# Optimization experiments

Measured on AMD Instinct MI355X. Metric: run time of the kernel, lower is better.

## Reference

```python
import jax, jax.numpy as jnp
import numpy as np

N_NODES = 50000
N_EDGES = 640000
IN_DIM, HID_DIM, OUT_DIM = 128, 128, 64


def setup_inputs() -> dict:
    key = jax.random.key(0)
    k = jax.random.split(key, 6)
    x = jax.random.normal(k[0], (N_NODES, IN_DIM), dtype=jnp.float32)
    edge_index = jax.random.randint(k[1], (2, N_EDGES), 0, N_NODES, dtype=jnp.int64)
    edge_weight = jax.random.uniform(k[2], (N_EDGES,), dtype=jnp.float32)
    W1 = jax.random.normal(k[3], (IN_DIM, HID_DIM), dtype=jnp.float32) / np.sqrt(IN_DIM)
    b1 = jnp.zeros((HID_DIM,), dtype=jnp.float32)
    W2 = jax.random.normal(k[4], (HID_DIM, OUT_DIM), dtype=jnp.float32) / np.sqrt(HID_DIM)
    b2 = jnp.zeros((OUT_DIM,), dtype=jnp.float32)
    return {"x": x, "edge_index": edge_index, "edge_weight": edge_weight,
            "W1": W1, "b1": b1, "W2": W2, "b2": b2}


def _gcn_norm(edge_index, edge_weight, num_nodes):
    # PyG gcn_norm: add self-loops (weight 1.0), then deg^-1/2 * w * deg^-1/2.
    loop = jnp.arange(num_nodes, dtype=edge_index.dtype)
    row = jnp.concatenate([edge_index[0], loop])
    col = jnp.concatenate([edge_index[1], loop])
    w = jnp.concatenate([edge_weight, jnp.ones((num_nodes,), edge_weight.dtype)])
    deg = jax.ops.segment_sum(w, col, num_segments=num_nodes)  # in-degree (flow source->target)
    dinv = jnp.where(deg > 0, jax.lax.rsqrt(deg), 0.0)
    norm = dinv[row] * w * dinv[col]
    return row, col, norm


def _gcn_conv(x, W, b, row, col, norm, num_nodes):
    h = x @ W                      # [N, d_out] small GEMM
    msg = h[row] * norm[:, None]   # [E+N, d_out] gather (memory-bound)
    out = jax.ops.segment_sum(msg, col, num_segments=num_nodes)  # scatter-add
    return out + b


def reference(x, edge_index, edge_weight, W1, b1, W2, b2):
    n = x.shape[0]
    row, col, norm = _gcn_norm(edge_index, edge_weight, n)
    h = jax.nn.relu(_gcn_conv(x, W1, b1, row, col, norm, n))
    h = _gcn_conv(h, W2, b2, row, col, norm, n)
    return h
```

## Files before the change

kernel.cpp:

```cpp
#include <hip/hip_runtime.h>
#include <hip/hip_bf16.h>
#include <cstdint>

#define N_NODES 50000
#define N_EDGES 640000
#define IN_DIM 128
#define HID_DIM 128
#define OUT_DIM 64

constexpr int EDGE_BLOCKS  = (N_EDGES + 255) / 256;
constexpr int SCAN_BLOCKS  = (N_NODES + 255) / 256;
constexpr int WSPLIT_ELEMS = 128 * (HID_DIM + OUT_DIM);

typedef __attribute__((ext_vector_type(8))) short bf16x8;
typedef __attribute__((ext_vector_type(4))) float f32x4;

static __device__ __forceinline__ ushort f32_bf16_rn(float f) {
    uint32_t u = __float_as_uint(f);
    u += 0x7fffu + ((u >> 16) & 1u);
    return (ushort)(u >> 16);
}
static __device__ __forceinline__ float bf16_f32(ushort h) {
    return __uint_as_float(((uint32_t)h) << 16);
}

static __device__ __forceinline__ int detect_i64(const void* p) {
    const int* q = (const int*)p;
    int odd_or = 0, even_or = 0;
#pragma unroll
    for (int i = 1; i < 64; i += 2) odd_or |= q[i];
#pragma unroll
    for (int i = 0; i < 64; i += 2) even_or |= q[i];
    return (odd_or == 0 && even_or != 0) ? 1 : 0;
}

__global__ void k_prep(unsigned long long* __restrict__ degcnt,
                       const float* __restrict__ W1, ushort* __restrict__ w1hi,
                       ushort* __restrict__ w1lo, const float* __restrict__ W2,
                       ushort* __restrict__ w2hi, ushort* __restrict__ w2lo) {
    int t = blockIdx.x * blockDim.x + threadIdx.x;
    if (t < N_NODES) degcnt[t] = 0ull;
    if (t >= WSPLIT_ELEMS) return;
    const float* W;
    ushort *whi, *wlo;
    int dout, tt = t;
    if (tt < 128 * HID_DIM) {
        W = W1; whi = w1hi; wlo = w1lo; dout = HID_DIM;
    } else {
        tt -= 128 * HID_DIM;
        W = W2; whi = w2hi; wlo = w2lo; dout = OUT_DIM;
    }
    int k = tt / dout, j = tt % dout;
    float w = W[tt];
    ushort hi = f32_bf16_rn(w);
    ushort lo = f32_bf16_rn(w - bf16_f32(hi));
    int nt = j >> 4, ks = k >> 5, g = (k >> 3) & 3, e = k & 7;
    int frag = (nt * 4 + ks) * 64 + g * 16 + (j & 15);
    whi[frag * 8 + e] = hi;
    wlo[frag * 8 + e] = lo;
}

__global__ void k_edges_rank(const void* __restrict__ ei, const float* __restrict__ w,
                             int* __restrict__ rows, int* __restrict__ cols,
                             int* __restrict__ rank,
                             unsigned long long* __restrict__ degcnt, int n_edges) {
    __shared__ int is64_s;
    if (threadIdx.x == 0) is64_s = detect_i64(ei);
    __syncthreads();
    int e = blockIdx.x * blockDim.x + threadIdx.x;
    if (e >= n_edges) return;
    int r, c;
    if (is64_s) {
        const long long* q = (const long long*)ei;
        r = (int)q[e];
        c = (int)q[e + n_edges];
    } else {
        const int* q = (const int*)ei;
        r = q[e];
        c = q[e + n_edges];
    }
    rows[e] = r;
    cols[e] = c;
    unsigned int wq = (unsigned int)rintf(w[e] * 16777216.0f);
    unsigned long long old = atomicAdd(&degcnt[c], (1ull << 32) | (unsigned long long)wq);
    rank[e] = (int)(old >> 32);
}

__global__ __launch_bounds__(256) void k_gemm1(const float* __restrict__ A,
                                               const ushort* __restrict__ whi_u,
                                               const ushort* __restrict__ wlo_u,
                                               ushort* __restrict__ C, int n) {
    constexpr int NT = HID_DIM / 16;
    const bf16x8* whi = (const bf16x8*)whi_u;
    const bf16x8* wlo = (const bf16x8*)wlo_u;
    int wave = threadIdx.x >> 6, lane = threadIdx.x & 63;
    int g = lane >> 4, rr = lane & 15;
    int row_base = blockIdx.x * 128 + wave * 32;

    f32x4 acc[2][NT];
#pragma unroll
    for (int mt = 0; mt < 2; ++mt)
#pragma unroll
        for (int nt = 0; nt < NT; ++nt) acc[mt][nt] = (f32x4){0.f, 0.f, 0.f, 0.f};

#pragma unroll
    for (int ks = 0; ks < 4; ++ks) {
        bf16x8 ahi[2], alo[2];
#pragma unroll
        for (int mt = 0; mt < 2; ++mt) {
            int row = row_base + mt * 16 + rr;
            float av[8];
            if (row < n) {
                const float* ap = &A[(size_t)row * IN_DIM + ks * 32 + g * 8];
                float4 p0 = *(const float4*)ap;
                float4 p1 = *(const float4*)(ap + 4);
                av[0] = p0.x; av[1] = p0.y; av[2] = p0.z; av[3] = p0.w;
                av[4] = p1.x; av[5] = p1.y; av[6] = p1.z; av[7] = p1.w;
            } else {
#pragma unroll
                for (int e = 0; e < 8; ++e) av[e] = 0.f;
            }
            union { bf16x8 v; ushort u[8]; } H, L;
#pragma unroll
            for (int e = 0; e < 8; ++e) {
                ushort h = f32_bf16_rn(av[e]);
                H.u[e] = h;
                L.u[e] = f32_bf16_rn(av[e] - bf16_f32(h));
            }
            ahi[mt] = H.v;
            alo[mt] = L.v;
        }
#pragma unroll
        for (int nt = 0; nt < NT; ++nt) {
            bf16x8 wh = whi[(nt * 4 + ks) * 64 + lane];
            bf16x8 wl = wlo[(nt * 4 + ks) * 64 + lane];
#pragma unroll
            for (int mt = 0; mt < 2; ++mt) {
                acc[mt][nt] = __builtin_amdgcn_mfma_f32_16x16x32_bf16(ahi[mt], wh, acc[mt][nt], 0, 0, 0);
                acc[mt][nt] = __builtin_amdgcn_mfma_f32_16x16x32_bf16(alo[mt], wh, acc[mt][nt], 0, 0, 0);
                acc[mt][nt] = __builtin_amdgcn_mfma_f32_16x16x32_bf16(ahi[mt], wl, acc[mt][nt], 0, 0, 0);
            }
        }
    }
#pragma unroll
    for (int mt = 0; mt < 2; ++mt) {
#pragma unroll
        for (int r = 0; r < 4; ++r) {
            int row = row_base + mt * 16 + g * 4 + r;
            if (row < n) {
#pragma unroll
                for (int nt = 0; nt < NT; ++nt)
                    C[(size_t)row * HID_DIM + nt * 16 + rr] = f32_bf16_rn(acc[mt][nt][r]);
            }
        }
    }
}

__global__ void k_scan_block(const unsigned long long* __restrict__ degcnt,
                             int* __restrict__ starts, int* __restrict__ bsums,
                             float* __restrict__ dinv, int n) {
    __shared__ int buf[256];
    int i = blockIdx.x * 256 + threadIdx.x;
    int v = 0;
    if (i < n) {
        unsigned long long dc = degcnt[i];
        v = (int)(dc >> 32);
        float deg = 1.0f + (float)(unsigned int)(dc & 0xffffffffu) * (1.0f / 16777216.0f);
        dinv[i] = rsqrtf(deg);
    }
    buf[threadIdx.x] = v;
    __syncthreads();
#pragma unroll
    for (int off = 1; off < 256; off <<= 1) {
        int t = (threadIdx.x >= off) ? buf[threadIdx.x - off] : 0;
        __syncthreads();
        buf[threadIdx.x] += t;
        __syncthreads();
    }
    if (i < n) starts[i] = buf[threadIdx.x] - v;
    if (threadIdx.x == 255) bsums[blockIdx.x] = buf[255];
}

__global__ void k_scan_tops(int* __restrict__ bsums, int nb) {
    __shared__ int buf[256];
    int v = (threadIdx.x < nb) ? bsums[threadIdx.x] : 0;
    buf[threadIdx.x] = v;
    __syncthreads();
#pragma unroll
    for (int off = 1; off < 256; off <<= 1) {
        int t = (threadIdx.x >= off) ? buf[threadIdx.x - off] : 0;
        __syncthreads();
        buf[threadIdx.x] += t;
        __syncthreads();
    }
    if (threadIdx.x < nb) bsums[threadIdx.x] = buf[threadIdx.x] - v;
}

__global__ void k_scan_add(int* __restrict__ starts, const int* __restrict__ bsums,
                           int n, int total) {
    int i = blockIdx.x * 256 + threadIdx.x;
    if (i < n) starts[i] += bsums[blockIdx.x];
    if (i == 0) starts[n] = total;
}

__global__ void k_fill(const int* __restrict__ rows, const int* __restrict__ cols,
                       const int* __restrict__ rank, const float* __restrict__ w,
                       const float* __restrict__ dinv, const int* __restrict__ starts,
                       int2* __restrict__ packed, int n_edges) {
    int e = blockIdx.x * blockDim.x + threadIdx.x;
    if (e >= n_edges) return;
    int r = rows[e], c = cols[e];
    float nm = dinv[r] * w[e] * dinv[c];
    int pos = starts[c] + rank[e];
    packed[pos] = make_int2(r, __float_as_int(nm));
}

template <int D>
__global__ void k_gather_b(const ushort* __restrict__ htmp, const int2* __restrict__ packed,
                           const int* __restrict__ starts, const float* __restrict__ dinv,
                           const float* __restrict__ bias, void* __restrict__ outv, int n) {
    int node = (int)((blockIdx.x * (size_t)blockDim.x + threadIdx.x) >> 6);
    if (node >= n) return;
    int lane = threadIdx.x & 63;
    int beg = __builtin_amdgcn_readfirstlane(starts[node]);
    int end = __builtin_amdgcn_readfirstlane(starts[node + 1]);
    float di = dinv[node];
    float s = di * di;

    if constexpr (D == 128) {
        uint us = ((const uint*)(htmp + (size_t)node * 128))[lane];
        float ax = bf16_f32((ushort)us) * s + bias[lane * 2];
        float ay = bf16_f32((ushort)(us >> 16)) * s + bias[lane * 2 + 1];
        for (int p0 = beg; p0 < end; p0 += 8) {
            int2 e[8];
#pragma unroll
            for (int u = 0; u < 8; ++u) {
                int p = p0 + u;
                e[u] = packed[p < end ? p : end - 1];
            }
            uint v[8];
#pragma unroll
            for (int u = 0; u < 8; ++u)
                v[u] = ((const uint*)(htmp + (size_t)e[u].x * 128))[lane];
#pragma unroll
            for (int u = 0; u < 8; ++u) {
                float nm = (p0 + u < end) ? __int_as_float(e[u].y) : 0.f;
                ax = fmaf(bf16_f32((ushort)v[u]), nm, ax);
                ay = fmaf(bf16_f32((ushort)(v[u] >> 16)), nm, ay);
            }
        }
        uint po = (uint)f32_bf16_rn(fmaxf(ax, 0.f)) | ((uint)f32_bf16_rn(fmaxf(ay, 0.f)) << 16);
        ((uint*)((ushort*)outv + (size_t)node * 128))[lane] = po;
    } else {
        float acc = bf16_f32(htmp[(size_t)node * 64 + lane]) * s + bias[lane];
        for (int p0 = beg; p0 < end; p0 += 8) {
            int2 e[8];
#pragma unroll
            for (int u = 0; u < 8; ++u) {
                int p = p0 + u;
                e[u] = packed[p < end ? p : end - 1];
            }
            float v[8];
#pragma unroll
            for (int u = 0; u < 8; ++u)
                v[u] = bf16_f32(htmp[(size_t)e[u].x * 64 + lane]);
#pragma unroll
            for (int u = 0; u < 8; ++u) {
                float nm = (p0 + u < end) ? __int_as_float(e[u].y) : 0.f;
                acc = fmaf(v[u], nm, acc);
            }
        }
        ((float*)outv)[(size_t)node * 64 + lane] = acc;
    }
}

__global__ __launch_bounds__(128) void k_gemm2(const ushort* __restrict__ A,
                                               const ushort* __restrict__ whi_u,
                                               const ushort* __restrict__ wlo_u,
                                               ushort* __restrict__ C, int n) {
    constexpr int NT = OUT_DIM / 16;
    const bf16x8* whi = (const bf16x8*)whi_u;
    const bf16x8* wlo = (const bf16x8*)wlo_u;
    int wave = threadIdx.x >> 6, lane = threadIdx.x & 63;
    int g = lane >> 4, rr = lane & 15;
    int row_base = blockIdx.x * 64 + wave * 32;

    f32x4 acc[2][NT];
#pragma unroll
    for (int mt = 0; mt < 2; ++mt)
#pragma unroll
        for (int nt = 0; nt < NT; ++nt) acc[mt][nt] = (f32x4){0.f, 0.f, 0.f, 0.f};

#pragma unroll
    for (int ks = 0; ks < 4; ++ks) {
        bf16x8 a[2];
#pragma unroll
        for (int mt = 0; mt < 2; ++mt) {
            int row = row_base + mt * 16 + rr;
            if (row < n)
                a[mt] = *(const bf16x8*)&A[(size_t)row * HID_DIM + ks * 32 + g * 8];
            else
                a[mt] = (bf16x8){0, 0, 0, 0, 0, 0, 0, 0};
        }
#pragma unroll
        for (int nt = 0; nt < NT; ++nt) {
            bf16x8 wh = whi[(nt * 4 + ks) * 64 + lane];
            bf16x8 wl = wlo[(nt * 4 + ks) * 64 + lane];
#pragma unroll
            for (int mt = 0; mt < 2; ++mt) {
                acc[mt][nt] = __builtin_amdgcn_mfma_f32_16x16x32_bf16(a[mt], wh, acc[mt][nt], 0, 0, 0);
                acc[mt][nt] = __builtin_amdgcn_mfma_f32_16x16x32_bf16(a[mt], wl, acc[mt][nt], 0, 0, 0);
            }
        }
    }
#pragma unroll
    for (int mt = 0; mt < 2; ++mt) {
#pragma unroll
        for (int r = 0; r < 4; ++r) {
            int row = row_base + mt * 16 + g * 4 + r;
            if (row < n) {
#pragma unroll
                for (int nt = 0; nt < NT; ++nt)
                    C[(size_t)row * OUT_DIM + nt * 16 + rr] = f32_bf16_rn(acc[mt][nt][r]);
            }
        }
    }
}

static inline size_t align_up(size_t x, size_t a) { return (x + a - 1) & ~(a - 1); }

extern "C" void kernel_launch(void* const* d_in, const int* in_sizes, int n_in,
                              void* d_out, int out_size, void* d_ws, size_t ws_size,
                              hipStream_t stream) {
    const float* x  = (const float*)d_in[0];
    const void*  ei = d_in[1];
    const float* ew = (const float*)d_in[2];
    const float* W1 = (const float*)d_in[3];
    const float* b1 = (const float*)d_in[4];
    const float* W2 = (const float*)d_in[5];
    const float* b2 = (const float*)d_in[6];
    float* out = (float*)d_out;

    const int N = N_NODES, E = N_EDGES;

    char* p = (char*)d_ws;
    int*    rows   = (int*)p;    p += align_up((size_t)E * 4, 512);
    int*    cols   = (int*)p;    p += align_up((size_t)E * 4, 512);
    int*    rank   = (int*)p;    p += align_up((size_t)E * 4, 512);
    unsigned long long* degcnt = (unsigned long long*)p; p += align_up((size_t)N * 8, 512);
    float*  dinv   = (float*)p;  p += align_up((size_t)N * 4, 512);
    int*    starts = (int*)p;    p += align_up((size_t)(N + 1) * 4, 512);
    int*    bsums  = (int*)p;    p += align_up((size_t)256 * 4, 512);
    int2*   packed = (int2*)p;   p += align_up((size_t)E * 8, 512);
    ushort* htmp1  = (ushort*)p; p += align_up((size_t)N * HID_DIM * 2, 512);
    ushort* h1     = (ushort*)p; p += align_up((size_t)N * HID_DIM * 2, 512);
    ushort* htmp2  = (ushort*)p; p += align_up((size_t)N * OUT_DIM * 2, 512);
    ushort* w1hi   = (ushort*)p; p += align_up((size_t)128 * HID_DIM * 2, 512);
    ushort* w1lo   = (ushort*)p; p += align_up((size_t)128 * HID_DIM * 2, 512);
    ushort* w2hi   = (ushort*)p; p += align_up((size_t)128 * OUT_DIM * 2, 512);
    ushort* w2lo   = (ushort*)p; p += align_up((size_t)128 * OUT_DIM * 2, 512);
    (void)ws_size;

    const int B = 256;
    int gE = (E + B - 1) / B;

    k_prep<<<SCAN_BLOCKS, B, 0, stream>>>(degcnt, W1, w1hi, w1lo, W2, w2hi, w2lo);

    k_edges_rank<<<EDGE_BLOCKS, B, 0, stream>>>(ei, ew, rows, cols, rank, degcnt, E);

    k_gemm1<<<(N + 127) / 128, 256, 0, stream>>>(x, w1hi, w1lo, htmp1, N);

    k_scan_block<<<SCAN_BLOCKS, 256, 0, stream>>>(degcnt, starts, bsums, dinv, N);
    k_scan_tops<<<1, 256, 0, stream>>>(bsums, SCAN_BLOCKS);
    k_scan_add<<<SCAN_BLOCKS, 256, 0, stream>>>(starts, bsums, N, E);
    k_fill<<<gE, B, 0, stream>>>(rows, cols, rank, ew, dinv, starts, packed, E);

    k_gather_b<HID_DIM><<<((size_t)N * 64 + B - 1) / B, B, 0, stream>>>(
        htmp1, packed, starts, dinv, b1, h1, N);

    k_gemm2<<<(N + 63) / 64, 128, 0, stream>>>(h1, w2hi, w2lo, htmp2, N);
    k_gather_b<OUT_DIM><<<((size_t)N * 64 + B - 1) / B, B, 0, stream>>>(
        htmp2, packed, starts, dinv, b2, out, N);
    (void)out_size; (void)n_in; (void)in_sizes;
}
```

Baseline: 140.8 us.

## Process two nodes per wavefront in gather and pack degree counters into 32 bits

The gather kernels now assign two destination nodes per 64-lane wavefront, 32 lanes each. Each lane loads wider vectors (uint2 for the 128-wide layer, uint for the 64-wide layer), which halves the number of wavefronts and raises the bytes fetched per load instruction. Edge bounds are no longer wave-uniform, so the edge loop can diverge between the two halves. Separately, the degree count and the quantized weight sum are packed into a 32-bit atomic (7-bit count, 25-bit fixed-point weight) instead of 64-bit. That lowers atomic width and precision, and it assumes in-degree stays below 128 and the weight sum fits the field.

```diff
diff --git a/kernel.cpp b/kernel.cpp
--- a/kernel.cpp
+++ b/kernel.cpp
@@ -34,12 +34,12 @@
     return (odd_or == 0 && even_or != 0) ? 1 : 0;
 }
 
-__global__ void k_prep(unsigned long long* __restrict__ degcnt,
+__global__ void k_prep(unsigned int* __restrict__ degcnt,
                        const float* __restrict__ W1, ushort* __restrict__ w1hi,
                        ushort* __restrict__ w1lo, const float* __restrict__ W2,
                        ushort* __restrict__ w2hi, ushort* __restrict__ w2lo) {
     int t = blockIdx.x * blockDim.x + threadIdx.x;
-    if (t < N_NODES) degcnt[t] = 0ull;
+    if (t < N_NODES) degcnt[t] = 0u;
     if (t >= WSPLIT_ELEMS) return;
     const float* W;
     ushort *whi, *wlo;
@@ -63,7 +63,7 @@
 __global__ void k_edges_rank(const void* __restrict__ ei, const float* __restrict__ w,
                              int* __restrict__ rows, int* __restrict__ cols,
                              int* __restrict__ rank,
-                             unsigned long long* __restrict__ degcnt, int n_edges) {
+                             unsigned int* __restrict__ degcnt, int n_edges) {
     __shared__ int is64_s;
     if (threadIdx.x == 0) is64_s = detect_i64(ei);
     __syncthreads();
@@ -81,9 +81,9 @@
     }
     rows[e] = r;
     cols[e] = c;
-    unsigned int wq = (unsigned int)rintf(w[e] * 16777216.0f);
-    unsigned long long old = atomicAdd(&degcnt[c], (1ull << 32) | (unsigned long long)wq);
-    rank[e] = (int)(old >> 32);
+    unsigned int wq = (unsigned int)rintf(w[e] * 524288.0f);
+    unsigned int old = atomicAdd(&degcnt[c], (1u << 25) + wq);
+    rank[e] = (int)(old >> 25);
 }
 
 __global__ __launch_bounds__(256) void k_gemm1(const float* __restrict__ A,
@@ -156,16 +156,16 @@
     }
 }
 
-__global__ void k_scan_block(const unsigned long long* __restrict__ degcnt,
+__global__ void k_scan_block(const unsigned int* __restrict__ degcnt,
                              int* __restrict__ starts, int* __restrict__ bsums,
                              float* __restrict__ dinv, int n) {
     __shared__ int buf[256];
     int i = blockIdx.x * 256 + threadIdx.x;
     int v = 0;
     if (i < n) {
-        unsigned long long dc = degcnt[i];
-        v = (int)(dc >> 32);
-        float deg = 1.0f + (float)(unsigned int)(dc & 0xffffffffu) * (1.0f / 16777216.0f);
+        unsigned int dc = degcnt[i];
+        v = (int)(dc >> 25);
+        float deg = 1.0f + (float)(dc & 0x1ffffffu) * (1.0f / 524288.0f);
         dinv[i] = rsqrtf(deg);
     }
     buf[threadIdx.x] = v;
@@ -219,18 +219,21 @@
 __global__ void k_gather_b(const ushort* __restrict__ htmp, const int2* __restrict__ packed,
                            const int* __restrict__ starts, const float* __restrict__ dinv,
                            const float* __restrict__ bias, void* __restrict__ outv, int n) {
-    int node = (int)((blockIdx.x * (size_t)blockDim.x + threadIdx.x) >> 6);
+    int wid = (int)((blockIdx.x * (size_t)blockDim.x + threadIdx.x) >> 6);
+    int lane = threadIdx.x & 63;
+    int half = lane >> 5, hl = lane & 31;
+    int node = wid * 2 + half;
     if (node >= n) return;
-    int lane = threadIdx.x & 63;
-    int beg = __builtin_amdgcn_readfirstlane(starts[node]);
-    int end = __builtin_amdgcn_readfirstlane(starts[node + 1]);
+    int beg = starts[node], end = starts[node + 1];
     float di = dinv[node];
     float s = di * di;
 
     if constexpr (D == 128) {
-        uint us = ((const uint*)(htmp + (size_t)node * 128))[lane];
-        float ax = bf16_f32((ushort)us) * s + bias[lane * 2];
-        float ay = bf16_f32((ushort)(us >> 16)) * s + bias[lane * 2 + 1];
+        uint2 us = ((const uint2*)(htmp + (size_t)node * 128))[hl];
+        float a0 = bf16_f32((ushort)us.x) * s + bias[4 * hl + 0];
+        float a1 = bf16_f32((ushort)(us.x >> 16)) * s + bias[4 * hl + 1];
+        float a2 = bf16_f32((ushort)us.y) * s + bias[4 * hl + 2];
+        float a3 = bf16_f32((ushort)(us.y >> 16)) * s + bias[4 * hl + 3];
         for (int p0 = beg; p0 < end; p0 += 8) {
             int2 e[8];
 #pragma unroll
@@ -238,21 +241,26 @@
                 int p = p0 + u;
                 e[u] = packed[p < end ? p : end - 1];
             }
-            uint v[8];
+            uint2 v[8];
 #pragma unroll
             for (int u = 0; u < 8; ++u)
-                v[u] = ((const uint*)(htmp + (size_t)e[u].x * 128))[lane];
+                v[u] = ((const uint2*)(htmp + (size_t)e[u].x * 128))[hl];
 #pragma unroll
             for (int u = 0; u < 8; ++u) {
                 float nm = (p0 + u < end) ? __int_as_float(e[u].y) : 0.f;
-                ax = fmaf(bf16_f32((ushort)v[u]), nm, ax);
-                ay = fmaf(bf16_f32((ushort)(v[u] >> 16)), nm, ay);
-            }
-        }
-        uint po = (uint)f32_bf16_rn(fmaxf(ax, 0.f)) | ((uint)f32_bf16_rn(fmaxf(ay, 0.f)) << 16);
-        ((uint*)((ushort*)outv + (size_t)node * 128))[lane] = po;
+                a0 = fmaf(bf16_f32((ushort)v[u].x), nm, a0);
+                a1 = fmaf(bf16_f32((ushort)(v[u].x >> 16)), nm, a1);
+                a2 = fmaf(bf16_f32((ushort)v[u].y), nm, a2);
+                a3 = fmaf(bf16_f32((ushort)(v[u].y >> 16)), nm, a3);
+            }
+        }
+        uint o0 = (uint)f32_bf16_rn(fmaxf(a0, 0.f)) | ((uint)f32_bf16_rn(fmaxf(a1, 0.f)) << 16);
+        uint o1 = (uint)f32_bf16_rn(fmaxf(a2, 0.f)) | ((uint)f32_bf16_rn(fmaxf(a3, 0.f)) << 16);
+        ((uint2*)((ushort*)outv + (size_t)node * 128))[hl] = make_uint2(o0, o1);
     } else {
-        float acc = bf16_f32(htmp[(size_t)node * 64 + lane]) * s + bias[lane];
+        uint us = ((const uint*)(htmp + (size_t)node * 64))[hl];
+        float a0 = bf16_f32((ushort)us) * s + bias[2 * hl + 0];
+        float a1 = bf16_f32((ushort)(us >> 16)) * s + bias[2 * hl + 1];
         for (int p0 = beg; p0 < end; p0 += 8) {
             int2 e[8];
 #pragma unroll
@@ -260,17 +268,18 @@
                 int p = p0 + u;
                 e[u] = packed[p < end ? p : end - 1];
             }
-            float v[8];
+            uint v[8];
 #pragma unroll
             for (int u = 0; u < 8; ++u)
-                v[u] = bf16_f32(htmp[(size_t)e[u].x * 64 + lane]);
+                v[u] = ((const uint*)(htmp + (size_t)e[u].x * 64))[hl];
 #pragma unroll
             for (int u = 0; u < 8; ++u) {
                 float nm = (p0 + u < end) ? __int_as_float(e[u].y) : 0.f;
-                acc = fmaf(v[u], nm, acc);
-            }
-        }
-        ((float*)outv)[(size_t)node * 64 + lane] = acc;
+                a0 = fmaf(bf16_f32((ushort)v[u]), nm, a0);
+                a1 = fmaf(bf16_f32((ushort)(v[u] >> 16)), nm, a1);
+            }
+        }
+        ((float2*)((float*)outv + (size_t)node * 64))[hl] = make_float2(a0, a1);
     }
 }
 
@@ -347,7 +356,7 @@
     int*    rows   = (int*)p;    p += align_up((size_t)E * 4, 512);
     int*    cols   = (int*)p;    p += align_up((size_t)E * 4, 512);
     int*    rank   = (int*)p;    p += align_up((size_t)E * 4, 512);
-    unsigned long long* degcnt = (unsigned long long*)p; p += align_up((size_t)N * 8, 512);
+    unsigned int* degcnt = (unsigned int*)p; p += align_up((size_t)N * 4, 512);
     float*  dinv   = (float*)p;  p += align_up((size_t)N * 4, 512);
     int*    starts = (int*)p;    p += align_up((size_t)(N + 1) * 4, 512);
     int*    bsums  = (int*)p;    p += align_up((size_t)256 * 4, 512);
@@ -363,6 +372,7 @@
 
     const int B = 256;
     int gE = (E + B - 1) / B;
+    int gather_blocks = (int)(((size_t)((N + 1) / 2) * 64 + B - 1) / B);
 
     k_prep<<<SCAN_BLOCKS, B, 0, stream>>>(degcnt, W1, w1hi, w1lo, W2, w2hi, w2lo);
 
@@ -375,11 +385,11 @@
     k_scan_add<<<SCAN_BLOCKS, 256, 0, stream>>>(starts, bsums, N, E);
     k_fill<<<gE, B, 0, stream>>>(rows, cols, rank, ew, dinv, starts, packed, E);
 
-    k_gather_b<HID_DIM><<<((size_t)N * 64 + B - 1) / B, B, 0, stream>>>(
+    k_gather_b<HID_DIM><<<gather_blocks, B, 0, stream>>>(
         htmp1, packed, starts, dinv, b1, h1, N);
 
     k_gemm2<<<(N + 63) / 64, 128, 0, stream>>>(h1, w2hi, w2lo, htmp2, N);
-    k_gather_b<OUT_DIM><<<((size_t)N * 64 + B - 1) / B, B, 0, stream>>>(
+    k_gather_b<OUT_DIM><<<gather_blocks, B, 0, stream>>>(
         htmp2, packed, starts, dinv, b2, out, N);
     (void)out_size; (void)n_in; (void)in_sizes;
 }
```

After: 141.7 us. Within noise of the previous version (+0.6%).

## Replicate degree counters across eight copies to cut atomic contention

Applied to the files above, without the earlier changes.

Replaces the single 64-bit packed count+weight atomic per node with 32-bit atomics spread over eight replicas chosen by thread index. Each replica packs a 7-bit count and a 25-bit fixed-point weight sum. The scan kernel combines the replicas into per-replica base offsets, and the fill kernel uses them to compute CSR positions. The aim is to lower atomic contention and use cheaper 32-bit atomics, at the cost of extra zeroing, more reads in the scan, a second base-offset array, and lower fixed-point precision for the weights. A node that collects 128 or more edges in one replica, or enough weight to carry past 25 bits, would overflow.

```diff
diff --git a/kernel.cpp b/kernel.cpp
--- a/kernel.cpp
+++ b/kernel.cpp
@@ -7,6 +7,7 @@
 #define IN_DIM 128
 #define HID_DIM 128
 #define OUT_DIM 64
+#define NREPL 8
 
 constexpr int EDGE_BLOCKS  = (N_EDGES + 255) / 256;
 constexpr int SCAN_BLOCKS  = (N_NODES + 255) / 256;
@@ -34,12 +35,15 @@
     return (odd_or == 0 && even_or != 0) ? 1 : 0;
 }
 
-__global__ void k_prep(unsigned long long* __restrict__ degcnt,
+__global__ void k_prep(unsigned int* __restrict__ degcnt_r,
                        const float* __restrict__ W1, ushort* __restrict__ w1hi,
                        ushort* __restrict__ w1lo, const float* __restrict__ W2,
                        ushort* __restrict__ w2hi, ushort* __restrict__ w2lo) {
     int t = blockIdx.x * blockDim.x + threadIdx.x;
-    if (t < N_NODES) degcnt[t] = 0ull;
+    if (t < N_NODES) {
+#pragma unroll
+        for (int r = 0; r < NREPL; ++r) degcnt_r[r * N_NODES + t] = 0u;
+    }
     if (t >= WSPLIT_ELEMS) return;
     const float* W;
     ushort *whi, *wlo;
@@ -63,7 +67,7 @@
 __global__ void k_edges_rank(const void* __restrict__ ei, const float* __restrict__ w,
                              int* __restrict__ rows, int* __restrict__ cols,
                              int* __restrict__ rank,
-                             unsigned long long* __restrict__ degcnt, int n_edges) {
+                             unsigned int* __restrict__ degcnt_r, int n_edges) {
     __shared__ int is64_s;
     if (threadIdx.x == 0) is64_s = detect_i64(ei);
     __syncthreads();
@@ -81,9 +85,10 @@
     }
     rows[e] = r;
     cols[e] = c;
-    unsigned int wq = (unsigned int)rintf(w[e] * 16777216.0f);
-    unsigned long long old = atomicAdd(&degcnt[c], (1ull << 32) | (unsigned long long)wq);
-    rank[e] = (int)(old >> 32);
+    int repl = threadIdx.x & (NREPL - 1);
+    unsigned int wq = (unsigned int)rintf(w[e] * 524288.0f);
+    unsigned int old = atomicAdd(&degcnt_r[repl * N_NODES + c], (1u << 25) + wq);
+    rank[e] = (repl << 26) | (int)(old >> 25);
 }
 
 __global__ __launch_bounds__(256) void k_gemm1(const float* __restrict__ A,
@@ -156,16 +161,25 @@
     }
 }
 
-__global__ void k_scan_block(const unsigned long long* __restrict__ degcnt,
+__global__ void k_scan_block(const unsigned int* __restrict__ degcnt_r,
                              int* __restrict__ starts, int* __restrict__ bsums,
+                             unsigned int* __restrict__ repl_base,
                              float* __restrict__ dinv, int n) {
     __shared__ int buf[256];
     int i = blockIdx.x * 256 + threadIdx.x;
     int v = 0;
     if (i < n) {
-        unsigned long long dc = degcnt[i];
-        v = (int)(dc >> 32);
-        float deg = 1.0f + (float)(unsigned int)(dc & 0xffffffffu) * (1.0f / 16777216.0f);
+        unsigned int wsum = 0;
+        unsigned int run = 0;
+#pragma unroll
+        for (int r = 0; r < NREPL; ++r) {
+            unsigned int dc = degcnt_r[r * N_NODES + i];
+            repl_base[r * N_NODES + i] = run;
+            run += dc >> 25;
+            wsum += dc & 0x1ffffffu;
+        }
+        v = (int)run;
+        float deg = 1.0f + (float)wsum * (1.0f / 524288.0f);
         dinv[i] = rsqrtf(deg);
     }
     buf[threadIdx.x] = v;
@@ -206,12 +220,15 @@
 __global__ void k_fill(const int* __restrict__ rows, const int* __restrict__ cols,
                        const int* __restrict__ rank, const float* __restrict__ w,
                        const float* __restrict__ dinv, const int* __restrict__ starts,
+                       const unsigned int* __restrict__ repl_base,
                        int2* __restrict__ packed, int n_edges) {
     int e = blockIdx.x * blockDim.x + threadIdx.x;
     if (e >= n_edges) return;
     int r = rows[e], c = cols[e];
+    int rk = rank[e];
+    int repl = (rk >> 26) & (NREPL - 1);
     float nm = dinv[r] * w[e] * dinv[c];
-    int pos = starts[c] + rank[e];
+    int pos = starts[c] + (int)repl_base[repl * N_NODES + c] + (rk & 0x3ffffff);
     packed[pos] = make_int2(r, __float_as_int(nm));
 }
 
@@ -347,7 +364,8 @@
     int*    rows   = (int*)p;    p += align_up((size_t)E * 4, 512);
     int*    cols   = (int*)p;    p += align_up((size_t)E * 4, 512);
     int*    rank   = (int*)p;    p += align_up((size_t)E * 4, 512);
-    unsigned long long* degcnt = (unsigned long long*)p; p += align_up((size_t)N * 8, 512);
+    unsigned int* degcnt_r = (unsigned int*)p; p += align_up((size_t)NREPL * N * 4, 512);
+    unsigned int* repl_base = (unsigned int*)p; p += align_up((size_t)NREPL * N * 4, 512);
     float*  dinv   = (float*)p;  p += align_up((size_t)N * 4, 512);
     int*    starts = (int*)p;    p += align_up((size_t)(N + 1) * 4, 512);
     int*    bsums  = (int*)p;    p += align_up((size_t)256 * 4, 512);
@@ -364,16 +382,16 @@
     const int B = 256;
     int gE = (E + B - 1) / B;
 
-    k_prep<<<SCAN_BLOCKS, B, 0, stream>>>(degcnt, W1, w1hi, w1lo, W2, w2hi, w2lo);
-
-    k_edges_rank<<<EDGE_BLOCKS, B, 0, stream>>>(ei, ew, rows, cols, rank, degcnt, E);
+    k_prep<<<SCAN_BLOCKS, B, 0, stream>>>(degcnt_r, W1, w1hi, w1lo, W2, w2hi, w2lo);
+
+    k_edges_rank<<<EDGE_BLOCKS, B, 0, stream>>>(ei, ew, rows, cols, rank, degcnt_r, E);
 
     k_gemm1<<<(N + 127) / 128, 256, 0, stream>>>(x, w1hi, w1lo, htmp1, N);
 
-    k_scan_block<<<SCAN_BLOCKS, 256, 0, stream>>>(degcnt, starts, bsums, dinv, N);
+    k_scan_block<<<SCAN_BLOCKS, 256, 0, stream>>>(degcnt_r, starts, bsums, repl_base, dinv, N);
     k_scan_tops<<<1, 256, 0, stream>>>(bsums, SCAN_BLOCKS);
     k_scan_add<<<SCAN_BLOCKS, 256, 0, stream>>>(starts, bsums, N, E);
-    k_fill<<<gE, B, 0, stream>>>(rows, cols, rank, ew, dinv, starts, packed, E);
+    k_fill<<<gE, B, 0, stream>>>(rows, cols, rank, ew, dinv, starts, repl_base, packed, E);
 
     k_gather_b<HID_DIM><<<((size_t)N * 64 + B - 1) / B, B, 0, stream>>>(
         htmp1, packed, starts, dinv, b1, h1, N);
```

After: 139.9 us. No clear change (-0.6%).
